# Performance work log

Measured on AMD Instinct MI355X. Metric: run time of the kernel, lower is better.

The kernel has to match this reference:

```python
import math
import jax, jax.numpy as jnp
import numpy as np

DIM = 3
NB = 8  # 2**DIM blades, grade-sorted: [1, e1, e2, e3, e12, e13, e23, e123]
GRADE_SLICES = [(0, 1), (1, 4), (4, 7), (7, 8)]
SUBSPACES = [1, 3, 3, 1]
GRADE_IDX = np.repeat(np.arange(4), SUBSPACES)  # blade -> grade index
EPS = 1e-6
SQRT2 = math.sqrt(2.0)


def _build_cayley():
    # Cl(3,0) Euclidean Cayley table, blades sorted by (grade, bitmask).
    masks = sorted(range(NB), key=lambda m: (bin(m).count("1"), m))
    pos = {m: i for i, m in enumerate(masks)}
    cay = np.zeros((NB, NB, NB), dtype=np.float32)
    for i, mi in enumerate(masks):
        for k, mk in enumerate(masks):
            a, s = mi >> 1, 0
            while a:
                s += bin(a & mk).count("1")
                a >>= 1
            cay[i, pos[mi ^ mk], k] = -1.0 if (s & 1) else 1.0
    triples = []
    for gi in range(4):
        for gj in range(4):
            for gk in range(4):
                (i0, i1), (j0, j1), (k0, k1) = GRADE_SLICES[gi], GRADE_SLICES[gj], GRADE_SLICES[gk]
                if np.any(cay[i0:i1, j0:j1, k0:k1] != 0):
                    triples.append((gi, gj, gk))
    return cay, triples

CAYLEY_NP, TRIPLES = _build_cayley()
NPATHS = len(TRIPLES)  # 20 nonzero grade-triple paths for Cl(3,0)


def mv_linear(x, w, b=None):
    # x: [B,n,8]; w: [m,n,4] (one weight per grade subspace); bias -> scalar blade only.
    w8 = w[..., GRADE_IDX]  # [m,n,8]
    out = jnp.einsum("bni,mni->bmi", x, w8)
    if b is not None:
        out = out.at[..., 0].add(b)
    return out


def grade_q(x):
    # per-grade squared magnitude (Euclidean metric -> all blade signs +1): [B,n,8]->[B,n,4]
    return jnp.stack([jnp.sum(x[..., s:e] ** 2, axis=-1) for s, e in GRADE_SLICES], axis=-1)


def normalization(x, a):
    # CGENN NormalizationLayer (init=0): interpolate per-grade norm toward 1 via sigmoid gate.
    norms = jnp.sqrt(grade_q(x))  # [B,n,4]
    sa = jax.nn.sigmoid(a)  # [n,4]
    norms = sa[None] * (norms - 1.0) + 1.0
    return x / (norms[..., GRADE_IDX] + EPS)


def mv_silu(x, a, b):
    # MVSiLU with invariant='mag2': gate on [scalar, q_grade1, q_grade2, q_grade3].
    q = grade_q(x)  # [B,n,4]
    inv = jnp.concatenate([x[..., :1], q[..., 1:]], axis=-1)  # [B,n,4]
    gate = a[None] * inv + b[None]
    return jax.nn.sigmoid(gate[..., GRADE_IDX]) * x


def fc_geometric_product(x, xr, w, cayley):
    # out[b,m,j] = sum_{n,i,k} x[b,n,i] * cayley[i,j,k] * W[m,n,path(gi,gj,gk)] * xr[b,n,k]
    B, n = x.shape[0], x.shape[1]
    m = w.shape[0]
    out = jnp.zeros((B, m, NB), dtype=x.dtype)
    for t, (gi, gj, gk) in enumerate(TRIPLES):
        (i0, i1), (j0, j1), (k0, k1) = GRADE_SLICES[gi], GRADE_SLICES[gj], GRADE_SLICES[gk]
        tmp = jnp.einsum("bni,ijk,bnk->bnj", x[..., i0:i1], cayley[i0:i1, j0:j1, k0:k1], xr[..., k0:k1])
        out = out.at[:, :, j0:j1].add(jnp.einsum("bnj,mn->bmj", tmp, w[:, :, t]))
    return out


def cw_geometric_product(x, xr, w, cayley):
    # channel-wise steerable GP: out[b,n,j] = sum_{i,k} x[b,n,i]*cayley[i,j,k]*w[n,path]*xr[b,n,k]
    out = jnp.zeros_like(x)
    for t, (gi, gj, gk) in enumerate(TRIPLES):
        (i0, i1), (j0, j1), (k0, k1) = GRADE_SLICES[gi], GRADE_SLICES[gj], GRADE_SLICES[gk]
        tmp = jnp.einsum("bni,ijk,bnk->bnj", x[..., i0:i1], cayley[i0:i1, j0:j1, k0:k1], xr[..., k0:k1])
        out = out.at[:, :, j0:j1].add(tmp * w[None, :, t, None])
    return out


B, IN, HID, OUT = 1024, 256, 512, 128


def setup_inputs():
    key = jax.random.key(0)
    ks = jax.random.split(key, 16)

    def nrm(k, shape, std):
        return jax.random.normal(k, shape, dtype=jnp.float32) * std

    s_in = 1.0 / math.sqrt(IN)
    s_hid = 1.0 / math.sqrt(HID)
    return {
        "x": jax.random.normal(ks[0], (B, IN, NB), dtype=jnp.float32),
        "lr1_w": nrm(ks[1], (IN, IN, 4), s_in),
        "n1_a": jnp.zeros((IN, 4), jnp.float32),
        "ll1_w": nrm(ks[2], (HID, IN, 4), s_in),
        "ll1_b": jnp.zeros((HID,), jnp.float32),
        "w1": nrm(ks[3], (HID, IN, NPATHS), 1.0 / math.sqrt(IN * (DIM + 1))),
        "act_a": jnp.ones((HID, 4), jnp.float32),
        "act_b": jnp.zeros((HID, 4), jnp.float32),
        "lrg_w": nrm(ks[4], (HID, HID, 4), s_hid),
        "ng_a": jnp.zeros((HID, 4), jnp.float32),
        "llg_w": nrm(ks[5], (HID, HID, 4), s_hid),
        "llg_b": jnp.zeros((HID,), jnp.float32),
        "wg": nrm(ks[6], (HID, NPATHS), 1.0 / math.sqrt(DIM + 1)),
        "lr2_w": nrm(ks[7], (HID, HID, 4), s_hid),
        "n2_a": jnp.zeros((HID, 4), jnp.float32),
        "ll2_w": nrm(ks[8], (OUT, HID, 4), s_hid),
        "ll2_b": jnp.zeros((OUT,), jnp.float32),
        "w2": nrm(ks[9], (OUT, HID, NPATHS), 1.0 / math.sqrt(HID * (DIM + 1))),
    }


def reference(x, lr1_w, n1_a, ll1_w, ll1_b, w1, act_a, act_b,
              lrg_w, ng_a, llg_w, llg_b, wg,
              lr2_w, n2_a, ll2_w, ll2_b, w2):
    cayley = jnp.asarray(CAYLEY_NP)
    # fcgp1: right linear -> normalize -> weighted geometric product + first-order term
    xr = normalization(mv_linear(x, lr1_w), n1_a)
    h = (mv_linear(x, ll1_w, ll1_b) + fc_geometric_product(x, xr, w1, cayley)) / SQRT2
    h = mv_silu(h, act_a, act_b)
    # channel-wise steerable geometric product layer
    hr = normalization(mv_linear(h, lrg_w), ng_a)
    h = (mv_linear(h, llg_w, llg_b) + cw_geometric_product(h, hr, wg, cayley)) / SQRT2
    h = mv_silu(h, act_a, act_b)
    # fcgp2
    hr = normalization(mv_linear(h, lr2_w), n2_a)
    out = (mv_linear(h, ll2_w, ll2_b) + fc_geometric_product(h, hr, w2, cayley)) / SQRT2
    return out
```

## Files before the change

### kernel.cpp

```cpp
#include <hip/hip_runtime.h>
#include <math.h>


typedef unsigned short u16;
typedef __attribute__((ext_vector_type(8))) short short8;
typedef __attribute__((ext_vector_type(4))) float f32x4;

#define RSQRT2F 0.70710678118654752440f

__device__ inline void gl_lds16(const void* g, void* l) {
  __builtin_amdgcn_global_load_lds(
      (const __attribute__((address_space(1))) void*)g,
      (__attribute__((address_space(3))) void*)l, 16, 0, 0);
}

__device__ constexpr int PP_I[64] = {
  0,0,0,0,0,0,0,0,  1,1,1,1,1,1,1,1,  2,2,2,2,2,2,2,2,  3,3,3,3,3,3,3,3,
  4,4,4,4,4,4,4,4,  5,5,5,5,5,5,5,5,  6,6,6,6,6,6,6,6,  7,7,7,7,7,7,7,7};
__device__ constexpr int PP_K[64] = {
  0,1,2,3,4,5,6,7,  0,1,2,3,4,5,6,7,  0,1,2,3,4,5,6,7,  0,1,2,3,4,5,6,7,
  0,1,2,3,4,5,6,7,  0,1,2,3,4,5,6,7,  0,1,2,3,4,5,6,7,  0,1,2,3,4,5,6,7};
__device__ constexpr int PP_C[64] = {
   0, 1, 2, 3, 4, 5, 6, 7,
   9, 8,15,16,13,14,21,20,
  10,15, 8,17,12,21,14,19,
  11,16,17, 8,21,12,13,18,
  29,24,23,35,22,34,33,28,
  30,25,35,23,34,22,32,27,
  31,35,25,24,33,32,22,26,
  43,42,41,40,39,38,37,36};
__device__ constexpr int PP_T[64] = {
   0, 1, 1, 1, 2, 2, 2, 3,
   5, 4, 7, 7, 6, 6, 9, 8,
   5, 7, 4, 7, 6, 9, 6, 8,
   5, 7, 7, 4, 9, 6, 6, 8,
  13,11,11,15,10,14,14,12,
  13,11,15,11,14,10,14,12,
  13,15,11,11,14,14,10,12,
  19,18,18,18,17,17,17,16};
__device__ constexpr int PP_J[64] = {
  0,1,2,3,4,5,6,7,
  1,0,4,5,2,3,7,6,
  2,4,0,6,1,7,3,5,
  3,5,6,0,7,1,2,4,
  4,2,1,7,0,6,5,3,
  5,3,7,1,6,0,4,2,
  6,7,3,2,5,4,0,1,
  7,6,5,4,3,2,1,0};
__device__ constexpr float PP_S[64] = {
  1, 1, 1, 1, 1, 1, 1, 1,
  1, 1, 1, 1, 1, 1, 1, 1,
  1,-1, 1, 1,-1,-1, 1,-1,
  1,-1,-1, 1, 1,-1,-1, 1,
  1,-1, 1, 1,-1,-1, 1,-1,
  1,-1,-1, 1, 1,-1,-1, 1,
  1, 1,-1, 1,-1, 1,-1,-1,
  1, 1,-1, 1,-1, 1,-1,-1};

__device__ constexpr int GJ_CNT[8] = {4,6,6,6,6,6,6,4};
__device__ constexpr int GJ_C[8][6] = {
  {0,8,22,36,0,0},
  {1,9,12,23,26,37},
  {2,10,13,24,27,38},
  {3,11,14,25,28,39},
  {4,15,18,29,32,40},
  {5,16,19,30,33,41},
  {6,17,20,31,34,42},
  {7,21,35,43,0,0}};
__device__ constexpr int GJ_T[8][6] = {
  {0,4,10,16,0,0},
  {1,5,6,11,12,17},
  {1,5,6,11,12,17},
  {1,5,6,11,12,17},
  {2,7,8,13,14,18},
  {2,7,8,13,14,18},
  {2,7,8,13,14,18},
  {3,9,15,19,0,0}};
__device__ constexpr int GRADE[8] = {0,1,1,1,2,2,2,3};

__device__ inline float sigm(float x) { return 1.0f / (1.0f + expf(-x)); }
__device__ inline u16 f2bf(float f) {
  unsigned u = __float_as_uint(f);
  return (u16)((u + 0x7fffu + ((u >> 16) & 1u)) >> 16);
}
__device__ inline float bf2f(u16 h) { return __uint_as_float(((unsigned)h) << 16); }

#define BT 128
#define MT 128
#define BKc 64

__global__ __launch_bounds__(256) void mfma_gemm(
    const u16* __restrict__ Alin, const u16* __restrict__ Pfeat,
    const u16* __restrict__ WLin, const u16* __restrict__ WLin2,
    const u16* __restrict__ WGp,
    float* __restrict__ out1, float* __restrict__ out2,
    int N, int M, int aug, int planeA, int planeO, int KSbits, int KCbits)
{
  const int zz    = blockIdx.z;
  const int set   = zz >> (3 + KSbits);
  const int rem   = zz & ((8 << KSbits) - 1);
  const int j     = rem >> KSbits;
  const int slice = rem & ((1 << KSbits) - 1);
  const u16* WL   = set ? WLin2 : WLin;
  float* outp     = set ? out2 : out1;

  const int b0   = blockIdx.y * BT;
  const int m0   = blockIdx.x * MT;
  const int tid  = threadIdx.x;
  const int lane = tid & 63;
  const int wave = tid >> 6;
  const int wr   = wave >> 1;
  const int wc   = wave & 1;
  const int l15  = lane & 15;
  const int lq   = lane >> 4;

  __shared__ u16 AsB[2][BT * BKc];
  __shared__ u16 BsB[2][MT * BKc];

  f32x4 zero = {0.f, 0.f, 0.f, 0.f};
  f32x4 acc[4][4];
  #pragma unroll
  for (int r = 0; r < 4; ++r)
    #pragma unroll
    for (int c = 0; c < 4; ++c) acc[r][c] = zero;

  const int g = GRADE[j];
  const int npass = aug ? (1 + GJ_CNT[j]) : 1;
  const int KC = 1 << KCbits;
  const int cper = (npass << KCbits) >> KSbits;
  const int cbeg = slice * cper;

  const int srow  = lane >> 3;
  const int sslot = lane & 7;

  {
    const int ci = cbeg;
    const int p  = ci >> KCbits;
    const int k0 = (ci & (KC - 1)) << 6;
    const u16* Ab = (p == 0) ? Alin + (size_t)j * planeA
                             : Pfeat + (size_t)GJ_C[j][p - 1] * planeA;
    const u16* Wb = (p == 0) ? WL + (size_t)g * M * N
                             : WGp + (size_t)GJ_T[j][p - 1] * (size_t)M * N;
    const u16* As0 = Ab + (size_t)b0 * N + k0;
    const u16* Bs0 = Wb + (size_t)m0 * N + k0;
    #pragma unroll
    for (int q = 0; q < 4; ++q) {
      int inst = wave * 4 + q, row = inst * 8 + srow;
      int kg = sslot ^ (row & 7);
      gl_lds16(As0 + (size_t)row * N + kg * 8, &AsB[0][inst * 512]);
    }
    #pragma unroll
    for (int q = 0; q < 4; ++q) {
      int inst = wave * 4 + q, row = inst * 8 + srow;
      int kg = sslot ^ (row & 7);
      gl_lds16(Bs0 + (size_t)row * N + kg * 8, &BsB[0][inst * 512]);
    }
  }

  #pragma unroll 1
  for (int ci = cbeg; ci < cbeg + cper; ++ci) {
    const int buf = (ci - cbeg) & 1;
    if (ci + 1 < cbeg + cper) {
      const int cn = ci + 1;
      const int p  = cn >> KCbits;
      const int k0 = (cn & (KC - 1)) << 6;
      const u16* Ab = (p == 0) ? Alin + (size_t)j * planeA
                               : Pfeat + (size_t)GJ_C[j][p - 1] * planeA;
      const u16* Wb = (p == 0) ? WL + (size_t)g * M * N
                               : WGp + (size_t)GJ_T[j][p - 1] * (size_t)M * N;
      const u16* As1 = Ab + (size_t)b0 * N + k0;
      const u16* Bs1 = Wb + (size_t)m0 * N + k0;
      #pragma unroll
      for (int q = 0; q < 4; ++q) {
        int inst = wave * 4 + q, row = inst * 8 + srow;
        int kg = sslot ^ (row & 7);
        gl_lds16(As1 + (size_t)row * N + kg * 8, &AsB[1 - buf][inst * 512]);
      }
      #pragma unroll
      for (int q = 0; q < 4; ++q) {
        int inst = wave * 4 + q, row = inst * 8 + srow;
        int kg = sslot ^ (row & 7);
        gl_lds16(Bs1 + (size_t)row * N + kg * 8, &BsB[1 - buf][inst * 512]);
      }
      asm volatile("s_waitcnt vmcnt(8)\n\ts_barrier" ::: "memory");
    } else {
      asm volatile("s_waitcnt vmcnt(0)\n\ts_barrier" ::: "memory");
    }

    const u16* As = &AsB[buf][0];
    const u16* Bs = &BsB[buf][0];
    #pragma unroll
    for (int s = 0; s < 2; ++s) {
      const int kq = s * 4 + lq;
      short8 af[4], bfr[4];
      #pragma unroll
      for (int r = 0; r < 4; ++r) {
        int row = wr * 64 + r * 16 + l15;
        af[r] = *(const short8*)(&As[row * BKc + (kq ^ (row & 7)) * 8]);
      }
      #pragma unroll
      for (int c = 0; c < 4; ++c) {
        int row = wc * 64 + c * 16 + l15;
        bfr[c] = *(const short8*)(&Bs[row * BKc + (kq ^ (row & 7)) * 8]);
      }
      #pragma unroll
      for (int r = 0; r < 4; ++r)
        #pragma unroll
        for (int c = 0; c < 4; ++c)
          acc[r][c] = __builtin_amdgcn_mfma_f32_16x16x32_bf16(af[r], bfr[c], acc[r][c], 0, 0, 0);
    }
    asm volatile("s_barrier" ::: "memory");
  }

  float* obase = outp + (size_t)(slice * 8 + j) * planeO;
  #pragma unroll
  for (int r = 0; r < 4; ++r)
    #pragma unroll
    for (int c = 0; c < 4; ++c)
      #pragma unroll
      for (int e = 0; e < 4; ++e) {
        int bb = b0 + wr * 64 + r * 16 + lq * 4 + e;
        int mm = m0 + wc * 64 + c * 16 + l15;
        obase[(size_t)bb * M + mm] = acc[r][c][e];
      }
}

struct RepackDesc { const float* in; u16* out; int MN; int S; };
struct RepackArgs { RepackDesc d[8]; const float* x; u16* xp; int PS; };

__global__ void repack_all(RepackArgs a)
{
  int mn = blockIdx.x * 256 + threadIdx.x;
  if (blockIdx.y == 8) {
    if (mn >= a.PS) return;
    float v[8];
    *(float4*)(v)     = *(const float4*)(a.x + (size_t)mn * 8);
    *(float4*)(v + 4) = *(const float4*)(a.x + (size_t)mn * 8 + 4);
    #pragma unroll
    for (int jj = 0; jj < 8; ++jj) a.xp[(size_t)jj * a.PS + mn] = f2bf(v[jj]);
    return;
  }
  RepackDesc d = a.d[blockIdx.y];
  if (mn >= d.MN) return;
  if (d.S == 4) {
    float4 v = ((const float4*)d.in)[mn];
    d.out[(size_t)0 * d.MN + mn] = f2bf(v.x);
    d.out[(size_t)1 * d.MN + mn] = f2bf(v.y);
    d.out[(size_t)2 * d.MN + mn] = f2bf(v.z);
    d.out[(size_t)3 * d.MN + mn] = f2bf(v.w);
  } else {
    #pragma unroll
    for (int q = 0; q < 5; ++q) {
      float4 v = *(const float4*)(d.in + (size_t)mn * 20 + q * 4);
      d.out[(size_t)(q * 4 + 0) * d.MN + mn] = f2bf(v.x);
      d.out[(size_t)(q * 4 + 1) * d.MN + mn] = f2bf(v.y);
      d.out[(size_t)(q * 4 + 2) * d.MN + mn] = f2bf(v.z);
      d.out[(size_t)(q * 4 + 3) * d.MN + mn] = f2bf(v.w);
    }
  }
}

__global__ void pair_norm_p(const u16* __restrict__ up, const float* __restrict__ vpart,
                            const float* __restrict__ na, u16* __restrict__ Pp,
                            int PS, int M, int KS)
{
  int t = blockIdx.x * 256 + threadIdx.x;
  if (t >= PS) return;
  int m = t % M;
  float u[8], v[8];
  #pragma unroll
  for (int jj = 0; jj < 8; ++jj) {
    u[jj] = bf2f(up[(size_t)jj * PS + t]);
    float s = 0.f;
    for (int sl = 0; sl < KS; ++sl) s += vpart[(size_t)(sl * 8 + jj) * PS + t];
    v[jj] = s;
  }
  float q[4];
  q[0] = sqrtf(v[0] * v[0]);
  q[1] = sqrtf(v[1] * v[1] + v[2] * v[2] + v[3] * v[3]);
  q[2] = sqrtf(v[4] * v[4] + v[5] * v[5] + v[6] * v[6]);
  q[3] = sqrtf(v[7] * v[7]);
  float sc[4];
  #pragma unroll
  for (int gg = 0; gg < 4; ++gg) {
    float sa = sigm(na[m * 4 + gg]);
    sc[gg] = 1.0f / (sa * (q[gg] - 1.0f) + 1.0f + 1e-6f);
  }
  #pragma unroll
  for (int jj = 0; jj < 8; ++jj) v[jj] *= sc[GRADE[jj]];
  float p[44];
  #pragma unroll
  for (int c = 0; c < 44; ++c) p[c] = 0.f;
  #pragma unroll
  for (int e = 0; e < 64; ++e)
    p[PP_C[e]] += PP_S[e] * u[PP_I[e]] * v[PP_K[e]];
  #pragma unroll
  for (int c = 0; c < 44; ++c) Pp[(size_t)c * PS + t] = f2bf(p[c]);
}

__global__ void bias_silu_p(const float* __restrict__ hpart, const float* __restrict__ bias,
                            const float* __restrict__ ga, const float* __restrict__ gb,
                            u16* __restrict__ sh, int PS, int M, int KS)
{
  int t = blockIdx.x * 256 + threadIdx.x;
  if (t >= PS) return;
  int m = t % M;
  float v[8];
  #pragma unroll
  for (int jj = 0; jj < 8; ++jj) {
    float s = 0.f;
    for (int sl = 0; sl < KS; ++sl) s += hpart[(size_t)(sl * 8 + jj) * PS + t];
    v[jj] = s;
  }
  v[0] += bias[m];
  #pragma unroll
  for (int jj = 0; jj < 8; ++jj) v[jj] *= RSQRT2F;
  float inv[4];
  inv[0] = v[0];
  inv[1] = v[1]*v[1] + v[2]*v[2] + v[3]*v[3];
  inv[2] = v[4]*v[4] + v[5]*v[5] + v[6]*v[6];
  inv[3] = v[7]*v[7];
  float gt[4];
  #pragma unroll
  for (int gg = 0; gg < 4; ++gg)
    gt[gg] = sigm(ga[m * 4 + gg] * inv[gg] + gb[m * 4 + gg]);
  #pragma unroll
  for (int jj = 0; jj < 8; ++jj)
    sh[(size_t)jj * PS + t] = f2bf(v[jj] * gt[GRADE[jj]]);
}

__global__ void cw_silu_p(const float* __restrict__ llg, const u16* __restrict__ up,
                          const float* __restrict__ hrraw, const float* __restrict__ na,
                          const float* __restrict__ wg, const float* __restrict__ bias,
                          const float* __restrict__ ga, const float* __restrict__ gb,
                          u16* __restrict__ sh, int PS, int M)
{
  int t = blockIdx.x * 256 + threadIdx.x;
  if (t >= PS) return;
  int n = t % M;
  float acc[8], u[8], v[8], w[20];
  #pragma unroll
  for (int jj = 0; jj < 8; ++jj) {
    acc[jj] = llg[(size_t)jj * PS + t];
    u[jj]   = bf2f(up[(size_t)jj * PS + t]);
    v[jj]   = hrraw[(size_t)jj * PS + t];
  }
  float q[4];
  q[0] = sqrtf(v[0] * v[0]);
  q[1] = sqrtf(v[1] * v[1] + v[2] * v[2] + v[3] * v[3]);
  q[2] = sqrtf(v[4] * v[4] + v[5] * v[5] + v[6] * v[6]);
  q[3] = sqrtf(v[7] * v[7]);
  float sc[4];
  #pragma unroll
  for (int gg = 0; gg < 4; ++gg) {
    float sa = sigm(na[n * 4 + gg]);
    sc[gg] = 1.0f / (sa * (q[gg] - 1.0f) + 1.0f + 1e-6f);
  }
  #pragma unroll
  for (int jj = 0; jj < 8; ++jj) v[jj] *= sc[GRADE[jj]];
  #pragma unroll
  for (int qq = 0; qq < 5; ++qq)
    *(float4*)(w + qq * 4) = *(const float4*)(wg + (size_t)n * 20 + qq * 4);
  acc[0] += bias[n];
  #pragma unroll
  for (int e = 0; e < 64; ++e)
    acc[PP_J[e]] += PP_S[e] * u[PP_I[e]] * v[PP_K[e]] * w[PP_T[e]];
  #pragma unroll
  for (int jj = 0; jj < 8; ++jj) acc[jj] *= RSQRT2F;
  float inv[4];
  inv[0] = acc[0];
  inv[1] = acc[1]*acc[1] + acc[2]*acc[2] + acc[3]*acc[3];
  inv[2] = acc[4]*acc[4] + acc[5]*acc[5] + acc[6]*acc[6];
  inv[3] = acc[7]*acc[7];
  float gt[4];
  #pragma unroll
  for (int gg = 0; gg < 4; ++gg)
    gt[gg] = sigm(ga[n * 4 + gg] * inv[gg] + gb[n * 4 + gg]);
  #pragma unroll
  for (int jj = 0; jj < 8; ++jj)
    sh[(size_t)jj * PS + t] = f2bf(acc[jj] * gt[GRADE[jj]]);
}

__global__ void final_p(const float* __restrict__ pre, const float* __restrict__ bias,
                        float* __restrict__ outp, int PS, int M, int KS)
{
  int t = blockIdx.x * 256 + threadIdx.x;
  if (t >= PS) return;
  int m = t % M;
  float v[8];
  #pragma unroll
  for (int jj = 0; jj < 8; ++jj) {
    float s = 0.f;
    for (int sl = 0; sl < KS; ++sl) s += pre[(size_t)(sl * 8 + jj) * PS + t];
    v[jj] = s;
  }
  v[0] += bias[m];
  #pragma unroll
  for (int jj = 0; jj < 8; ++jj) v[jj] *= RSQRT2F;
  *(float4*)(outp + (size_t)t * 8)     = *(float4*)(v);
  *(float4*)(outp + (size_t)t * 8 + 4) = *(float4*)(v + 4);
}

extern "C" void kernel_launch(void* const* d_in, const int* in_sizes, int n_in,
                              void* d_out, int out_size, void* d_ws, size_t ws_size,
                              hipStream_t stream)
{
  const float* x     = (const float*)d_in[0];
  const float* lr1_w = (const float*)d_in[1];
  const float* n1_a  = (const float*)d_in[2];
  const float* ll1_w = (const float*)d_in[3];
  const float* ll1_b = (const float*)d_in[4];
  const float* w1    = (const float*)d_in[5];
  const float* act_a = (const float*)d_in[6];
  const float* act_b = (const float*)d_in[7];
  const float* lrg_w = (const float*)d_in[8];
  const float* ng_a  = (const float*)d_in[9];
  const float* llg_w = (const float*)d_in[10];
  const float* llg_b = (const float*)d_in[11];
  const float* wg    = (const float*)d_in[12];
  const float* lr2_w = (const float*)d_in[13];
  const float* n2_a  = (const float*)d_in[14];
  const float* ll2_w = (const float*)d_in[15];
  const float* ll2_b = (const float*)d_in[16];
  const float* w2    = (const float*)d_in[17];
  float* out = (float*)d_out;

  u16* W = (u16*)d_ws;
  size_t o = 0;
  u16* WL1  = W + o; o +=  262144;
  u16* WLL1 = W + o; o +=  524288;
  u16* WG1  = W + o; o += 2621440;
  u16* WLRG = W + o; o += 1048576;
  u16* WLLG = W + o; o += 1048576;
  u16* WLR2 = W + o; o += 1048576;
  u16* WLL2 = W + o; o +=  262144;
  u16* WG2  = W + o; o += 1310720;
  u16* XB   = W + o; o += 2097152;
  u16* HB   = W + o; o += 4194304;
  u16* P    = W + o; o += 23068672;
  float* f1 = (float*)(W + o);
  float* f2 = f1 + 8388608;
  float* hrP  = f2;
  float* llgP = f2 + 4194304;

  dim3 blk(256);
  const int PS1 = 1024 * 256, PS2 = 1024 * 512, PSO = 1024 * 128;

  RepackArgs ra = {{
    {lr1_w, WL1, 65536, 4}, {ll1_w, WLL1, 131072, 4}, {w1, WG1, 131072, 20},
    {lrg_w, WLRG, 262144, 4}, {llg_w, WLLG, 262144, 4}, {lr2_w, WLR2, 262144, 4},
    {ll2_w, WLL2, 65536, 4}, {w2, WG2, 65536, 20}},
    x, XB, PS1};
  repack_all<<<dim3(1024, 9), blk, 0, stream>>>(ra);

  mfma_gemm<<<dim3(2, 8, 16), blk, 0, stream>>>(XB, nullptr, WL1, nullptr, nullptr,
      f1, nullptr, 256, 256, 0, PS1, PS1, 1, 2);
  pair_norm_p<<<PS1 / 256, blk, 0, stream>>>(XB, f1, n1_a, P, PS1, 256, 2);
  mfma_gemm<<<dim3(4, 8, 16), blk, 0, stream>>>(XB, P, WLL1, nullptr, WG1,
      f1, nullptr, 256, 512, 1, PS1, PS2, 1, 2);
  bias_silu_p<<<PS2 / 256, blk, 0, stream>>>(f1, ll1_b, act_a, act_b, HB, PS2, 512, 2);

  mfma_gemm<<<dim3(4, 8, 16), blk, 0, stream>>>(HB, nullptr, WLRG, WLLG, nullptr,
      hrP, llgP, 512, 512, 0, PS2, PS2, 0, 3);
  cw_silu_p<<<PS2 / 256, blk, 0, stream>>>(llgP, HB, hrP, ng_a, wg, llg_b, act_a, act_b,
      HB, PS2, 512);

  mfma_gemm<<<dim3(4, 8, 16), blk, 0, stream>>>(HB, nullptr, WLR2, nullptr, nullptr,
      f1, nullptr, 512, 512, 0, PS2, PS2, 1, 3);
  pair_norm_p<<<PS2 / 256, blk, 0, stream>>>(HB, f1, n2_a, P, PS2, 512, 2);
  mfma_gemm<<<dim3(1, 8, 64), blk, 0, stream>>>(HB, P, WLL2, nullptr, WG2,
      f1, nullptr, 512, 128, 1, PS2, PSO, 3, 3);
  final_p<<<PSO / 256, blk, 0, stream>>>(f1, ll2_b, out, PSO, 128, 8);
}
```

Before: 258.3 us.

## Store intermediate GEMM split-K partials in bf16 and halve final split-K

Adds an out16 flag so the MFMA GEMM epilogue can write bf16 instead of fp32. The intermediate partial outputs consumed by pair_norm, bias_silu and cw_silu are now read as bf16, halving write and read traffic. The last GEMM drops from 8 to 4 K-slices, so final_p reduces fewer fp32 partials. Rounding split-K partials to bf16 before summing adds precision error, and the stores are 2-byte scattered writes, which may coalesce poorly.

```diff
diff --git a/kernel.cpp b/kernel.cpp
--- a/kernel.cpp
+++ b/kernel.cpp
@@ -93,8 +93,9 @@
     const u16* __restrict__ Alin, const u16* __restrict__ Pfeat,
     const u16* __restrict__ WLin, const u16* __restrict__ WLin2,
     const u16* __restrict__ WGp,
-    float* __restrict__ out1, float* __restrict__ out2,
-    int N, int M, int aug, int planeA, int planeO, int KSbits, int KCbits)
+    void* __restrict__ out1, void* __restrict__ out2,
+    int N, int M, int aug, int planeA, int planeO, int KSbits, int KCbits,
+    int out16)
 {
   const int zz    = blockIdx.z;
   const int set   = zz >> (3 + KSbits);
@@ -102,7 +103,7 @@
   const int j     = rem >> KSbits;
   const int slice = rem & ((1 << KSbits) - 1);
   const u16* WL   = set ? WLin2 : WLin;
-  float* outp     = set ? out2 : out1;
+  void* outp      = set ? out2 : out1;
 
   const int b0   = blockIdx.y * BT;
   const int m0   = blockIdx.x * MT;
@@ -212,7 +213,7 @@
     asm volatile("s_barrier" ::: "memory");
   }
 
-  float* obase = outp + (size_t)(slice * 8 + j) * planeO;
+  const size_t po = (size_t)(slice * 8 + j) * planeO;
   #pragma unroll
   for (int r = 0; r < 4; ++r)
     #pragma unroll
@@ -221,7 +222,8 @@
       for (int e = 0; e < 4; ++e) {
         int bb = b0 + wr * 64 + r * 16 + lq * 4 + e;
         int mm = m0 + wc * 64 + c * 16 + l15;
-        obase[(size_t)bb * M + mm] = acc[r][c][e];
+        if (out16) ((u16*)outp)[po + (size_t)bb * M + mm] = f2bf(acc[r][c][e]);
+        else       ((float*)outp)[po + (size_t)bb * M + mm] = acc[r][c][e];
       }
 }
 
@@ -260,7 +262,7 @@
   }
 }
 
-__global__ void pair_norm_p(const u16* __restrict__ up, const float* __restrict__ vpart,
+__global__ void pair_norm_p(const u16* __restrict__ up, const u16* __restrict__ vpart,
                             const float* __restrict__ na, u16* __restrict__ Pp,
                             int PS, int M, int KS)
 {
@@ -272,7 +274,7 @@
   for (int jj = 0; jj < 8; ++jj) {
     u[jj] = bf2f(up[(size_t)jj * PS + t]);
     float s = 0.f;
-    for (int sl = 0; sl < KS; ++sl) s += vpart[(size_t)(sl * 8 + jj) * PS + t];
+    for (int sl = 0; sl < KS; ++sl) s += bf2f(vpart[(size_t)(sl * 8 + jj) * PS + t]);
     v[jj] = s;
   }
   float q[4];
@@ -298,7 +300,7 @@
   for (int c = 0; c < 44; ++c) Pp[(size_t)c * PS + t] = f2bf(p[c]);
 }
 
-__global__ void bias_silu_p(const float* __restrict__ hpart, const float* __restrict__ bias,
+__global__ void bias_silu_p(const u16* __restrict__ hpart, const float* __restrict__ bias,
                             const float* __restrict__ ga, const float* __restrict__ gb,
                             u16* __restrict__ sh, int PS, int M, int KS)
 {
@@ -309,7 +311,7 @@
   #pragma unroll
   for (int jj = 0; jj < 8; ++jj) {
     float s = 0.f;
-    for (int sl = 0; sl < KS; ++sl) s += hpart[(size_t)(sl * 8 + jj) * PS + t];
+    for (int sl = 0; sl < KS; ++sl) s += bf2f(hpart[(size_t)(sl * 8 + jj) * PS + t]);
     v[jj] = s;
   }
   v[0] += bias[m];
@@ -329,8 +331,8 @@
     sh[(size_t)jj * PS + t] = f2bf(v[jj] * gt[GRADE[jj]]);
 }
 
-__global__ void cw_silu_p(const float* __restrict__ llg, const u16* __restrict__ up,
-                          const float* __restrict__ hrraw, const float* __restrict__ na,
+__global__ void cw_silu_p(const u16* __restrict__ llg, const u16* __restrict__ up,
+                          const u16* __restrict__ hrraw, const float* __restrict__ na,
                           const float* __restrict__ wg, const float* __restrict__ bias,
                           const float* __restrict__ ga, const float* __restrict__ gb,
                           u16* __restrict__ sh, int PS, int M)
@@ -341,9 +343,9 @@
   float acc[8], u[8], v[8], w[20];
   #pragma unroll
   for (int jj = 0; jj < 8; ++jj) {
-    acc[jj] = llg[(size_t)jj * PS + t];
+    acc[jj] = bf2f(llg[(size_t)jj * PS + t]);
     u[jj]   = bf2f(up[(size_t)jj * PS + t]);
-    v[jj]   = hrraw[(size_t)jj * PS + t];
+    v[jj]   = bf2f(hrraw[(size_t)jj * PS + t]);
   }
   float q[4];
   q[0] = sqrtf(v[0] * v[0]);
@@ -438,10 +440,10 @@
   u16* XB   = W + o; o += 2097152;
   u16* HB   = W + o; o += 4194304;
   u16* P    = W + o; o += 23068672;
+  u16* PB16 = W + o; o += 8388608;
+  u16* hr16  = W + o; o += 4194304;
+  u16* llg16 = W + o; o += 4194304;
   float* f1 = (float*)(W + o);
-  float* f2 = f1 + 8388608;
-  float* hrP  = f2;
-  float* llgP = f2 + 4194304;
 
   dim3 blk(256);
   const int PS1 = 1024 * 256, PS2 = 1024 * 512, PSO = 1024 * 128;
@@ -454,21 +456,21 @@
   repack_all<<<dim3(1024, 9), blk, 0, stream>>>(ra);
 
   mfma_gemm<<<dim3(2, 8, 16), blk, 0, stream>>>(XB, nullptr, WL1, nullptr, nullptr,
-      f1, nullptr, 256, 256, 0, PS1, PS1, 1, 2);
-  pair_norm_p<<<PS1 / 256, blk, 0, stream>>>(XB, f1, n1_a, P, PS1, 256, 2);
+      PB16, nullptr, 256, 256, 0, PS1, PS1, 1, 2, 1);
+  pair_norm_p<<<PS1 / 256, blk, 0, stream>>>(XB, PB16, n1_a, P, PS1, 256, 2);
   mfma_gemm<<<dim3(4, 8, 16), blk, 0, stream>>>(XB, P, WLL1, nullptr, WG1,
-      f1, nullptr, 256, 512, 1, PS1, PS2, 1, 2);
-  bias_silu_p<<<PS2 / 256, blk, 0, stream>>>(f1, ll1_b, act_a, act_b, HB, PS2, 512, 2);
+      PB16, nullptr, 256, 512, 1, PS1, PS2, 1, 2, 1);
+  bias_silu_p<<<PS2 / 256, blk, 0, stream>>>(PB16, ll1_b, act_a, act_b, HB, PS2, 512, 2);
 
   mfma_gemm<<<dim3(4, 8, 16), blk, 0, stream>>>(HB, nullptr, WLRG, WLLG, nullptr,
-      hrP, llgP, 512, 512, 0, PS2, PS2, 0, 3);
-  cw_silu_p<<<PS2 / 256, blk, 0, stream>>>(llgP, HB, hrP, ng_a, wg, llg_b, act_a, act_b,
+      hr16, llg16, 512, 512, 0, PS2, PS2, 0, 3, 1);
+  cw_silu_p<<<PS2 / 256, blk, 0, stream>>>(llg16, HB, hr16, ng_a, wg, llg_b, act_a, act_b,
       HB, PS2, 512);
 
   mfma_gemm<<<dim3(4, 8, 16), blk, 0, stream>>>(HB, nullptr, WLR2, nullptr, nullptr,
-      f1, nullptr, 512, 512, 0, PS2, PS2, 1, 3);
-  pair_norm_p<<<PS2 / 256, blk, 0, stream>>>(HB, f1, n2_a, P, PS2, 512, 2);
-  mfma_gemm<<<dim3(1, 8, 64), blk, 0, stream>>>(HB, P, WLL2, nullptr, WG2,
-      f1, nullptr, 512, 128, 1, PS2, PSO, 3, 3);
-  final_p<<<PSO / 256, blk, 0, stream>>>(f1, ll2_b, out, PSO, 128, 8);
-}
+      PB16, nullptr, 512, 512, 0, PS2, PS2, 1, 3, 1);
+  pair_norm_p<<<PS2 / 256, blk, 0, stream>>>(HB, PB16, n2_a, P, PS2, 512, 2);
+  mfma_gemm<<<dim3(1, 8, 32), blk, 0, stream>>>(HB, P, WLL2, nullptr, WG2,
+      f1, nullptr, 512, 128, 1, PS2, PSO, 2, 3, 0);
+  final_p<<<PSO / 256, blk, 0, stream>>>(f1, ll2_b, out, PSO, 128, 4);
+}
```

Measured after the change: 253.0 us. 1.02x faster.
